# Kernel tuning notes

Measured on AMD Instinct MI355X. Metric: run time of the kernel, lower is better.

The kernel has to match this reference:

```python
import jax, jax.numpy as jnp
import numpy as np

DIM = 512
EDIM = 2 * DIM          # edim(=2) * dim
OUT_DIM = 512
KERNEL_SIZE = 4096
B, L = 4, 4096


def setup_inputs() -> dict:
    key = jax.random.key(0)
    k0, k1, k2, k3, k4 = jax.random.split(key, 5)
    embeddings = jax.random.normal(k0, (B, L, DIM), dtype=jnp.float32)
    logit_alpha = jax.random.uniform(k1, (EDIM,), minval=-3.0, maxval=3.0, dtype=jnp.float32)
    logit_delta = jax.random.uniform(k2, (EDIM,), minval=-3.0, maxval=3.0, dtype=jnp.float32)
    # xavier_uniform: U(-a, a), a = sqrt(6/(fan_in+fan_out))
    a_beta = float(np.sqrt(6.0 / (DIM + EDIM)))
    beta = jax.random.uniform(k3, (DIM, EDIM), minval=-a_beta, maxval=a_beta, dtype=jnp.float32)
    a_eta = float(np.sqrt(6.0 / (EDIM + OUT_DIM)))
    eta = jax.random.uniform(k4, (EDIM, OUT_DIM), minval=-a_eta, maxval=a_eta, dtype=jnp.float32)
    return {"embeddings": embeddings, "logit_alpha": logit_alpha,
            "logit_delta": logit_delta, "beta": beta, "eta": eta}


def reference(embeddings, logit_alpha, logit_delta, beta, eta):
    K = KERNEL_SIZE
    Lseq = embeddings.shape[1]
    # data-dependent EMA decay kernel: kernel[e, t] = p_e * q_e^t
    alpha = jax.nn.sigmoid(logit_alpha)[:, None]            # [E, 1]
    delta = jax.nn.sigmoid(logit_delta)[:, None]            # [E, 1]
    p = alpha
    q = 1.0 - alpha * delta
    len_range = jnp.arange(K, dtype=embeddings.dtype)[None, :]   # [1, K]
    kernel = p * jnp.exp(jnp.log(q) * len_range)            # [E, K]

    u = jnp.einsum('bld,de->ble', embeddings, beta)         # [B, L, E]
    u_T = jnp.swapaxes(u, -1, -2)                           # [B, E, L]

    # forward (causal) direction: flip kernel, full conv via FFT, slice at K-1
    kernel_f = jnp.flip(kernel, axis=-1)
    fft_dim = Lseq + K
    fft_dim = 1 << (fft_dim - 1).bit_length()               # next power of 2 (static)
    inp_fft = jnp.fft.rfft(u_T, n=fft_dim, axis=-1)
    ker_fft = jnp.fft.rfft(kernel_f, n=fft_dim, axis=-1)    # [E, fft_dim//2+1]
    out_full = jnp.fft.irfft(inp_fft * ker_fft, n=fft_dim, axis=-1)
    out_T = out_full[..., K - 1:K - 1 + Lseq].astype(embeddings.dtype)  # [B, E, L]

    out = jnp.swapaxes(out_T, -1, -2)                       # [B, L, E]
    return jnp.einsum('ble,eo->blo', out, eta)              # [B, L, out_dim]
```

## Files before the change

kernel.cpp:

```cpp
#include <hip/hip_runtime.h>
#include <hip/hip_bf16.h>

#define DIM      512
#define EDIM     1024
#define OUTD     512
#define BATCH    4
#define LSEQ     4096
#define MROWS    (BATCH * LSEQ)
#define NCHUNK   16
#define CHUNK    (LSEQ / NCHUNK)

typedef __attribute__((ext_vector_type(8))) __bf16 bf16x8;
typedef __attribute__((ext_vector_type(4))) float  f32x4;

static __device__ __forceinline__ ushort f2b(float f) {
    uint x = __float_as_uint(f);
    x += 0x7fff + ((x >> 16) & 1);
    return (ushort)(x >> 16);
}
static __device__ __forceinline__ float b2f(ushort u) {
    return __uint_as_float(((uint)u) << 16);
}
static __device__ __forceinline__ float sigmoidf(float x) {
    return 1.0f / (1.0f + expf(-x));
}

__global__ void prep_kernel(const float* __restrict__ beta,
                            const float* __restrict__ eta,
                            const float* __restrict__ la,
                            const float* __restrict__ ld,
                            ushort* __restrict__ betaT,
                            ushort* __restrict__ etaT,
                            float* __restrict__ p,
                            float* __restrict__ q) {
    int i = blockIdx.x * blockDim.x + threadIdx.x;
    if (i < EDIM * DIM) {
        int n = i / DIM, k = i - n * DIM;
        betaT[i] = f2b(beta[(size_t)k * EDIM + n]);
    }
    if (i < OUTD * EDIM) {
        int o = i / EDIM, e = i - o * EDIM;
        etaT[i] = f2b(eta[(size_t)e * OUTD + o]);
    }
    if (i < EDIM) {
        float a = sigmoidf(la[i]);
        float d = sigmoidf(ld[i]);
        p[i] = a;
        q[i] = 1.0f - a * d;
    }
}

__global__ void cvt_emb_kernel(const float* __restrict__ emb,
                               ushort* __restrict__ a16) {
    int i = blockIdx.x * blockDim.x + threadIdx.x;
    float4 v = ((const float4*)emb)[i];
    ushort4 o;
    o.x = f2b(v.x); o.y = f2b(v.y); o.z = f2b(v.z); o.w = f2b(v.w);
    ((ushort4*)a16)[i] = o;
}

template <int OUT_BF16>
__global__ __launch_bounds__(256) void gemm_bt(const ushort* __restrict__ A,
                                               const ushort* __restrict__ Bt,
                                               void* __restrict__ Cv,
                                               int M, int N, int K) {
    __shared__ ushort smem[16384];
    const int tid  = threadIdx.x;
    const int lane = tid & 63;
    const int wid  = tid >> 6;
    const int wr   = wid >> 1, wc = wid & 1;
    const int l15  = lane & 15;
    const int l4   = lane >> 4;
    const int rowBase = blockIdx.x * 128;
    const int colBase = blockIdx.y * 128;

    f32x4 acc[4][4] = {};

    const int nkb = K >> 6;
    for (int kb = 0; kb < nkb; ++kb) {
        #pragma unroll
        for (int r = 0; r < 4; ++r) {
            int c     = r * 256 + tid;
            int row   = c >> 3;
            int col16 = (c & 7) ^ (row & 7);
            const ushort* ga = A  + (size_t)(rowBase + row) * K + kb * 64 + col16 * 8;
            __builtin_amdgcn_global_load_lds(
                (const __attribute__((address_space(1))) void*)ga,
                (__attribute__((address_space(3))) void*)((char*)smem + c * 16),
                16, 0, 0);
            const ushort* gb = Bt + (size_t)(colBase + row) * K + kb * 64 + col16 * 8;
            __builtin_amdgcn_global_load_lds(
                (const __attribute__((address_space(1))) void*)gb,
                (__attribute__((address_space(3))) void*)((char*)smem + 16384 + c * 16),
                16, 0, 0);
        }
        __syncthreads();

        #pragma unroll
        for (int kk = 0; kk < 2; ++kk) {
            bf16x8 af[4], bfr[4];
            #pragma unroll
            for (int m = 0; m < 4; ++m) {
                int row   = wr * 64 + m * 16 + l15;
                int kbyte = kk * 64 + l4 * 16;
                int addr  = row * 128 + (kbyte ^ ((row & 7) << 4));
                af[m] = *(const bf16x8*)((const char*)smem + addr);
            }
            #pragma unroll
            for (int n = 0; n < 4; ++n) {
                int row   = wc * 64 + n * 16 + l15;
                int kbyte = kk * 64 + l4 * 16;
                int addr  = 16384 + row * 128 + (kbyte ^ ((row & 7) << 4));
                bfr[n] = *(const bf16x8*)((const char*)smem + addr);
            }
            #pragma unroll
            for (int m = 0; m < 4; ++m)
                #pragma unroll
                for (int n = 0; n < 4; ++n)
                    acc[m][n] = __builtin_amdgcn_mfma_f32_16x16x32_bf16(
                        af[m], bfr[n], acc[m][n], 0, 0, 0);
        }
        __syncthreads();
    }

    #pragma unroll
    for (int m = 0; m < 4; ++m)
        #pragma unroll
        for (int n = 0; n < 4; ++n)
            #pragma unroll
            for (int r = 0; r < 4; ++r) {
                int row = rowBase + wr * 64 + m * 16 + l4 * 4 + r;
                int col = colBase + wc * 64 + n * 16 + l15;
                if (OUT_BF16)
                    ((ushort*)Cv)[(size_t)row * N + col] = f2b(acc[m][n][r]);
                else
                    ((float*)Cv)[(size_t)row * N + col] = acc[m][n][r];
            }
}

__global__ void scan_agg_kernel(const ushort* __restrict__ u,
                                const float* __restrict__ qv,
                                float* __restrict__ agg) {
    int t = blockIdx.x * blockDim.x + threadIdx.x;
    int e = t & (EDIM - 1);
    int g = t >> 10;
    int b = g >> 4;
    int c = g & 15;
    float qe = qv[e];
    const ushort* up = u + (size_t)(b * LSEQ + c * CHUNK) * EDIM + e;
    float acc = 0.0f, w = 1.0f;
    #pragma unroll 8
    for (int j = 0; j < CHUNK; ++j) {
        acc += w * b2f(up[(size_t)j * EDIM]);
        w *= qe;
    }
    agg[t] = acc;
}

__global__ void scan_apply_kernel(ushort* __restrict__ u,
                                  const float* __restrict__ pv,
                                  const float* __restrict__ qv,
                                  const float* __restrict__ agg) {
    int t = blockIdx.x * blockDim.x + threadIdx.x;
    int e = t & (EDIM - 1);
    int g = t >> 10;
    int b = g >> 4;
    int c = g & 15;
    float qe = qv[e], pe = pv[e];
    float qL = qe;
    #pragma unroll
    for (int s = 0; s < 8; ++s) qL *= qL;
    float carry = 0.0f, w = 1.0f;
    for (int cp = c + 1; cp < NCHUNK; ++cp) {
        carry += w * agg[((b * NCHUNK + cp) << 10) + e];
        w *= qL;
    }
    ushort* up = u + (size_t)(b * LSEQ + c * CHUNK) * EDIM + e;
    float S = carry;
    #pragma unroll 8
    for (int j = CHUNK - 1; j >= 0; --j) {
        S = b2f(up[(size_t)j * EDIM]) + qe * S;
        up[(size_t)j * EDIM] = f2b(pe * S);
    }
}

extern "C" void kernel_launch(void* const* d_in, const int* in_sizes, int n_in,
                              void* d_out, int out_size, void* d_ws, size_t ws_size,
                              hipStream_t stream) {
    const float* emb  = (const float*)d_in[0];
    const float* la   = (const float*)d_in[1];
    const float* ld   = (const float*)d_in[2];
    const float* beta = (const float*)d_in[3];
    const float* eta  = (const float*)d_in[4];

    char* ws = (char*)d_ws;
    ushort* a16   = (ushort*)(ws);
    ushort* betaT = (ushort*)(ws + 16777216);
    ushort* etaT  = (ushort*)(ws + 17825792);
    ushort* u     = (ushort*)(ws + 18874368);
    float*  p     = (float*) (ws + 52428800);
    float*  q     = (float*) (ws + 52432896);
    float*  agg   = (float*) (ws + 52436992);

    prep_kernel<<<dim3(2048), dim3(256), 0, stream>>>(beta, eta, la, ld,
                                                      betaT, etaT, p, q);
    cvt_emb_kernel<<<dim3(8192), dim3(256), 0, stream>>>(emb, a16);

    gemm_bt<1><<<dim3(MROWS / 128, EDIM / 128), dim3(256), 0, stream>>>(
        a16, betaT, (void*)u, MROWS, EDIM, DIM);

    scan_agg_kernel<<<dim3(256), dim3(256), 0, stream>>>(u, q, agg);
    scan_apply_kernel<<<dim3(256), dim3(256), 0, stream>>>(u, p, q, agg);

    gemm_bt<0><<<dim3(MROWS / 128, OUTD / 128), dim3(256), 0, stream>>>(
        u, etaT, d_out, MROWS, OUTD, EDIM);
}
```

Measured before the change: 99.11 us.

## Fuse chunk aggregate into first GEMM epilogue, merge prep kernels, remap GEMM grid

New measurement: 87.28 us. -11.9%, faster.

```diff
diff --git a/kernel.cpp b/kernel.cpp
--- a/kernel.cpp
+++ b/kernel.cpp
@@ -7,7 +7,7 @@
 #define BATCH    4
 #define LSEQ     4096
 #define MROWS    (BATCH * LSEQ)
-#define NCHUNK   16
+#define NCHUNK   64
 #define CHUNK    (LSEQ / NCHUNK)
 
 typedef __attribute__((ext_vector_type(8))) __bf16 bf16x8;
@@ -25,45 +25,50 @@
     return 1.0f / (1.0f + expf(-x));
 }
 
-__global__ void prep_kernel(const float* __restrict__ beta,
-                            const float* __restrict__ eta,
-                            const float* __restrict__ la,
-                            const float* __restrict__ ld,
-                            ushort* __restrict__ betaT,
-                            ushort* __restrict__ etaT,
-                            float* __restrict__ p,
-                            float* __restrict__ q) {
-    int i = blockIdx.x * blockDim.x + threadIdx.x;
-    if (i < EDIM * DIM) {
-        int n = i / DIM, k = i - n * DIM;
-        betaT[i] = f2b(beta[(size_t)k * EDIM + n]);
-    }
-    if (i < OUTD * EDIM) {
-        int o = i / EDIM, e = i - o * EDIM;
-        etaT[i] = f2b(eta[(size_t)e * OUTD + o]);
-    }
-    if (i < EDIM) {
-        float a = sigmoidf(la[i]);
-        float d = sigmoidf(ld[i]);
-        p[i] = a;
-        q[i] = 1.0f - a * d;
-    }
-}
-
-__global__ void cvt_emb_kernel(const float* __restrict__ emb,
-                               ushort* __restrict__ a16) {
-    int i = blockIdx.x * blockDim.x + threadIdx.x;
-    float4 v = ((const float4*)emb)[i];
-    ushort4 o;
-    o.x = f2b(v.x); o.y = f2b(v.y); o.z = f2b(v.z); o.w = f2b(v.w);
-    ((ushort4*)a16)[i] = o;
-}
-
-template <int OUT_BF16>
+__global__ void prep_cvt_kernel(const float* __restrict__ emb,
+                                ushort* __restrict__ a16,
+                                const float* __restrict__ beta,
+                                const float* __restrict__ eta,
+                                const float* __restrict__ la,
+                                const float* __restrict__ ld,
+                                ushort* __restrict__ betaT,
+                                ushort* __restrict__ etaT,
+                                float* __restrict__ p,
+                                float* __restrict__ q) {
+    int blk = blockIdx.x;
+    if (blk < 8192) {
+        int i = blk * 256 + threadIdx.x;
+        float4 v = ((const float4*)emb)[i];
+        ushort4 o;
+        o.x = f2b(v.x); o.y = f2b(v.y); o.z = f2b(v.z); o.w = f2b(v.w);
+        ((ushort4*)a16)[i] = o;
+    } else {
+        int i = (blk - 8192) * 256 + threadIdx.x;
+        if (i < EDIM * DIM) {
+            int n = i / DIM, k = i - n * DIM;
+            betaT[i] = f2b(beta[(size_t)k * EDIM + n]);
+        }
+        if (i < OUTD * EDIM) {
+            int o = i / EDIM, e = i - o * EDIM;
+            etaT[i] = f2b(eta[(size_t)e * OUTD + o]);
+        }
+        if (i < EDIM) {
+            float a = sigmoidf(la[i]);
+            float d = sigmoidf(ld[i]);
+            p[i] = a;
+            q[i] = 1.0f - a * d;
+        }
+    }
+}
+
+template <int OUT_BF16, int DO_AGG>
 __global__ __launch_bounds__(256) void gemm_bt(const ushort* __restrict__ A,
                                                const ushort* __restrict__ Bt,
                                                void* __restrict__ Cv,
-                                               int M, int N, int K) {
+                                               const float* __restrict__ qv,
+                                               float* __restrict__ aggp,
+                                               int M, int N, int K,
+                                               int ncolShift) {
     __shared__ ushort smem[16384];
     const int tid  = threadIdx.x;
     const int lane = tid & 63;
@@ -71,8 +76,12 @@
     const int wr   = wid >> 1, wc = wid & 1;
     const int l15  = lane & 15;
     const int l4   = lane >> 4;
-    const int rowBase = blockIdx.x * 128;
-    const int colBase = blockIdx.y * 128;
+
+    const int nwg   = gridDim.x;
+    const int chunkw = nwg >> 3;
+    const int flat  = (blockIdx.x & 7) * chunkw + (blockIdx.x >> 3);
+    const int rowBase = (flat >> ncolShift) << 7;
+    const int colBase = (flat & ((1 << ncolShift) - 1)) << 7;
 
     f32x4 acc[4][4] = {};
 
@@ -136,25 +145,30 @@
                 else
                     ((float*)Cv)[(size_t)row * N + col] = acc[m][n][r];
             }
-}
-
-__global__ void scan_agg_kernel(const ushort* __restrict__ u,
-                                const float* __restrict__ qv,
-                                float* __restrict__ agg) {
-    int t = blockIdx.x * blockDim.x + threadIdx.x;
-    int e = t & (EDIM - 1);
-    int g = t >> 10;
-    int b = g >> 4;
-    int c = g & 15;
-    float qe = qv[e];
-    const ushort* up = u + (size_t)(b * LSEQ + c * CHUNK) * EDIM + e;
-    float acc = 0.0f, w = 1.0f;
-    #pragma unroll 8
-    for (int j = 0; j < CHUNK; ++j) {
-        acc += w * b2f(up[(size_t)j * EDIM]);
-        w *= qe;
-    }
-    agg[t] = acc;
+
+    if (DO_AGG) {
+        const int bidx     = rowBase >> 12;
+        const int chunkIdx = ((rowBase & 4095) >> 6) + wr;
+        #pragma unroll
+        for (int n = 0; n < 4; ++n) {
+            int col = colBase + wc * 64 + n * 16 + l15;
+            float qe = qv[col];
+            float q2 = qe * qe, q4 = q2 * q2, q8 = q4 * q4, q16 = q8 * q8;
+            float P = 0.0f;
+            #pragma unroll
+            for (int m = 3; m >= 0; --m) {
+                f32x4 a = acc[m][n];
+                float pm = ((a[3] * qe + a[2]) * qe + a[1]) * qe + a[0];
+                P = P * q16 + pm;
+            }
+            float ql4 = (l4 & 1 ? q4 : 1.0f) * (l4 & 2 ? q8 : 1.0f);
+            P *= ql4;
+            P += __shfl_xor(P, 16, 64);
+            P += __shfl_xor(P, 32, 64);
+            if (l4 == 0)
+                aggp[(((bidx << 6) | chunkIdx) << 10) + col] = P;
+        }
+    }
 }
 
 __global__ void scan_apply_kernel(ushort* __restrict__ u,
@@ -162,25 +176,36 @@
                                   const float* __restrict__ qv,
                                   const float* __restrict__ agg) {
     int t = blockIdx.x * blockDim.x + threadIdx.x;
-    int e = t & (EDIM - 1);
-    int g = t >> 10;
-    int b = g >> 4;
-    int c = g & 15;
-    float qe = qv[e], pe = pv[e];
-    float qL = qe;
+    int e0 = (t & 511) * 2;
+    int c  = (t >> 9) & 63;
+    int b  = t >> 15;
+    float2 qe2 = *(const float2*)(qv + e0);
+    float2 pe2 = *(const float2*)(pv + e0);
+    float qe[2] = {qe2.x, qe2.y};
+    float pe[2] = {pe2.x, pe2.y};
+    float qL[2], S[2], w[2];
     #pragma unroll
-    for (int s = 0; s < 8; ++s) qL *= qL;
-    float carry = 0.0f, w = 1.0f;
+    for (int k = 0; k < 2; ++k) {
+        float x = qe[k];
+        #pragma unroll
+        for (int s = 0; s < 6; ++s) x *= x;
+        qL[k] = x; S[k] = 0.0f; w[k] = 1.0f;
+    }
     for (int cp = c + 1; cp < NCHUNK; ++cp) {
-        carry += w * agg[((b * NCHUNK + cp) << 10) + e];
-        w *= qL;
-    }
-    ushort* up = u + (size_t)(b * LSEQ + c * CHUNK) * EDIM + e;
-    float S = carry;
-    #pragma unroll 8
+        float2 a = *(const float2*)(agg + (((b << 6) | cp) << 10) + e0);
+        S[0] += w[0] * a.x;  w[0] *= qL[0];
+        S[1] += w[1] * a.y;  w[1] *= qL[1];
+    }
+    ushort* up = u + ((size_t)(b * LSEQ + c * CHUNK) << 10) + e0;
+    #pragma unroll 4
     for (int j = CHUNK - 1; j >= 0; --j) {
-        S = b2f(up[(size_t)j * EDIM]) + qe * S;
-        up[(size_t)j * EDIM] = f2b(pe * S);
+        ushort2 uv = *(ushort2*)(up + (size_t)j * EDIM);
+        S[0] = b2f(uv.x) + qe[0] * S[0];
+        S[1] = b2f(uv.y) + qe[1] * S[1];
+        ushort2 ov;
+        ov.x = f2b(pe[0] * S[0]);
+        ov.y = f2b(pe[1] * S[1]);
+        *(ushort2*)(up + (size_t)j * EDIM) = ov;
     }
 }
 
@@ -202,16 +227,14 @@
     float*  q     = (float*) (ws + 52432896);
     float*  agg   = (float*) (ws + 52436992);
 
-    prep_kernel<<<dim3(2048), dim3(256), 0, stream>>>(beta, eta, la, ld,
-                                                      betaT, etaT, p, q);
-    cvt_emb_kernel<<<dim3(8192), dim3(256), 0, stream>>>(emb, a16);
-
-    gemm_bt<1><<<dim3(MROWS / 128, EDIM / 128), dim3(256), 0, stream>>>(
-        a16, betaT, (void*)u, MROWS, EDIM, DIM);
-
-    scan_agg_kernel<<<dim3(256), dim3(256), 0, stream>>>(u, q, agg);
-    scan_apply_kernel<<<dim3(256), dim3(256), 0, stream>>>(u, p, q, agg);
-
-    gemm_bt<0><<<dim3(MROWS / 128, OUTD / 128), dim3(256), 0, stream>>>(
-        u, etaT, d_out, MROWS, OUTD, EDIM);
-}
+    prep_cvt_kernel<<<dim3(10240), dim3(256), 0, stream>>>(
+        emb, a16, beta, eta, la, ld, betaT, etaT, p, q);
+
+    gemm_bt<1, 1><<<dim3((MROWS / 128) * (EDIM / 128)), dim3(256), 0, stream>>>(
+        a16, betaT, (void*)u, q, agg, MROWS, EDIM, DIM, 3);
+
+    scan_apply_kernel<<<dim3(512), dim3(256), 0, stream>>>(u, p, q, agg);
+
+    gemm_bt<0, 0><<<dim3((MROWS / 128) * (OUTD / 128)), dim3(256), 0, stream>>>(
+        u, etaT, d_out, nullptr, nullptr, MROWS, OUTD, EDIM, 2);
+}
```
